# Kernel optimization log

Measured on AMD Instinct MI355X. Metric: run time of the kernel, lower is better.

The kernel has to match this reference:

```python
import jax, jax.numpy as jnp
import numpy as np

FONT_NUM = 190
HID = 256
HEADS = 2
EPS = 1e-5


def _bn(x, g, b, m, v):
    # eval-mode BatchNorm over the last (channel) axis
    return (x - m) * (g * jax.lax.rsqrt(v + EPS)) + b


def _gru(x, Wih, Whh, bih, bhh):
    # x: [B, S, D]; PyTorch gate order r, z, n. Returns all hidden states [B, S, H].
    B, S, _ = x.shape
    H = Whh.shape[1]
    xp = x @ Wih.T + bih  # [B, S, 3H] -- one big GEMM for all timesteps
    def step(h, xt):
        gh = h @ Whh.T + bhh
        xr, xz, xn = jnp.split(xt, 3, axis=-1)
        hr, hz, hn = jnp.split(gh, 3, axis=-1)
        r = jax.nn.sigmoid(xr + hr)
        z = jax.nn.sigmoid(xz + hz)
        n = jnp.tanh(xn + r * hn)
        h_new = (1.0 - z) * n + z * h
        return h_new, h_new
    h0 = jnp.zeros((B, H), x.dtype)
    _, hs = jax.lax.scan(step, h0, jnp.swapaxes(xp, 0, 1))
    return jnp.swapaxes(hs, 0, 1)


def _forward(img_emb, text_embs, len_mask, label_mask, labels,
             img_W, img_b, img_g, img_beta, img_m, img_v,
             g1_Wih, g1_Whh, g1_bih, g1_bhh, tl_W, tl_b,
             t_g, t_beta, t_m, t_v,
             g2_Wih, g2_Whh, g2_bih, g2_bhh, cl_W, cl_b,
             c_g, c_beta, c_m, c_v,
             attn_Win, attn_bin, attn_Wout, attn_bout, pred_W, pred_b):
    # img encoder: Linear -> BN -> (Dropout eval=id) -> ReLU
    img_fea = jax.nn.relu(_bn(img_emb @ img_W.T + img_b, img_g, img_beta, img_m, img_v))  # [B,H]
    # text encoder: GRU -> ReLU -> Linear, then BN+ReLU (torch does this in [B,C,S]; equivalent over channels)
    t = jax.nn.relu(_gru(text_embs, g1_Wih, g1_Whh, g1_bih, g1_bhh))
    t = t @ tl_W.T + tl_b
    text_fea = jax.nn.relu(_bn(t, t_g, t_beta, t_m, t_v))  # [B,S,H]
    len_info = len_mask.sum(axis=1)  # [B]
    # NOTE: sum over ALL timesteps divided by valid length (faithful to source)
    mean = text_fea.sum(axis=1) / len_info[:, None]  # [B,H]
    contrast = text_fea - mean[:, None, :]
    c = jax.nn.relu(_gru(contrast, g2_Wih, g2_Whh, g2_bih, g2_bhh))
    c = c @ cl_W.T + cl_b
    contrast_fea = jax.nn.relu(_bn(c, c_g, c_beta, c_m, c_v))  # [B,S,H]
    B, S, H = text_fea.shape
    hd = H // HEADS
    # batched 3-token self-attention: collapse the per-timestep python loop into one call
    tokens = jnp.stack([
        jnp.broadcast_to(img_fea[:, None, :], (B, S, H)), text_fea, contrast_fea
    ], axis=0).reshape(3, B * S, H)  # [3, N, H]
    Wq, Wk, Wv = jnp.split(attn_Win, 3, axis=0)
    bq, bk, bv = jnp.split(attn_bin, 3, axis=0)
    scale = 1.0 / jnp.sqrt(jnp.asarray(hd, tokens.dtype))
    q = (tokens @ Wq.T + bq).reshape(3, B * S, HEADS, hd) * scale
    k = (tokens @ Wk.T + bk).reshape(3, B * S, HEADS, hd)
    v = (tokens @ Wv.T + bv).reshape(3, B * S, HEADS, hd)
    scores = jnp.einsum('tnhd,snhd->nhts', q, k)  # [N, heads, 3, 3]
    attn = jax.nn.softmax(scores, axis=-1)
    o = jnp.einsum('nhts,snhd->tnhd', attn, v).reshape(3, B * S, H)
    o = o @ attn_Wout.T + attn_bout
    last = o.mean(axis=0).reshape(B, S, H)  # att_fea.mean(0) over the 3 tokens
    logits = last @ pred_W.T + pred_b  # [B,S,FONT_NUM]
    pred = jax.nn.softmax(logits, axis=-1)
    oh = jnp.maximum(label_mask, jax.nn.one_hot(labels, FONT_NUM, dtype=pred.dtype))
    loss = -(oh * jnp.log(pred)).sum(axis=-1)  # [B,S]
    loss = (loss * len_mask).sum(axis=1) / len_info
    return loss.mean()


def setup_inputs() -> dict:
    key = jax.random.key(0)
    ks = jax.random.split(key, 16)
    B, S, D, H = 128, 128, 2048, HID
    img_emb = jax.random.normal(ks[0], (B, D), jnp.float32)
    text_embs = jax.random.normal(ks[1], (B, S, D), jnp.float32)
    lengths = jax.random.randint(ks[2], (B,), S // 2, S + 1)
    len_mask = (jnp.arange(S)[None, :] < lengths[:, None]).astype(jnp.float32)
    labels = jax.random.randint(ks[3], (B, S), 0, FONT_NUM)
    label_mask = jnp.zeros((B, S, FONT_NUM), jnp.float32)
    w = lambda k, sh: jax.random.normal(k, sh, jnp.float32) * 0.02
    params = dict(
        img_W=w(ks[4], (H, D)), img_b=jnp.zeros((H,)),
        img_g=jnp.ones((H,)), img_beta=jnp.zeros((H,)), img_m=jnp.zeros((H,)), img_v=jnp.ones((H,)),
        g1_Wih=w(ks[5], (3 * (H // 2), D)), g1_Whh=w(ks[6], (3 * (H // 2), H // 2)),
        g1_bih=jnp.zeros((3 * (H // 2),)), g1_bhh=jnp.zeros((3 * (H // 2),)),
        tl_W=w(ks[7], (H, H // 2)), tl_b=jnp.zeros((H,)),
        t_g=jnp.ones((H,)), t_beta=jnp.zeros((H,)), t_m=jnp.zeros((H,)), t_v=jnp.ones((H,)),
        g2_Wih=w(ks[8], (3 * H, H)), g2_Whh=w(ks[9], (3 * H, H)),
        g2_bih=jnp.zeros((3 * H,)), g2_bhh=jnp.zeros((3 * H,)),
        cl_W=w(ks[10], (H, H)), cl_b=jnp.zeros((H,)),
        c_g=jnp.ones((H,)), c_beta=jnp.zeros((H,)), c_m=jnp.zeros((H,)), c_v=jnp.ones((H,)),
        attn_Win=w(ks[11], (3 * H, H)), attn_bin=jnp.zeros((3 * H,)),
        attn_Wout=w(ks[12], (H, H)), attn_bout=jnp.zeros((H,)),
        pred_W=w(ks[13], (FONT_NUM, H)), pred_b=jnp.zeros((FONT_NUM,)),
    )
    return dict(img_emb=img_emb, text_embs=text_embs, len_mask=len_mask,
                label_mask=label_mask, labels=labels, **params)


def reference(img_emb, text_embs, len_mask, label_mask, labels,
              img_W, img_b, img_g, img_beta, img_m, img_v,
              g1_Wih, g1_Whh, g1_bih, g1_bhh, tl_W, tl_b,
              t_g, t_beta, t_m, t_v,
              g2_Wih, g2_Whh, g2_bih, g2_bhh, cl_W, cl_b,
              c_g, c_beta, c_m, c_v,
              attn_Win, attn_bin, attn_Wout, attn_bout, pred_W, pred_b):
    return _forward(img_emb, text_embs, len_mask, label_mask, labels,
                    img_W, img_b, img_g, img_beta, img_m, img_v,
                    g1_Wih, g1_Whh, g1_bih, g1_bhh, tl_W, tl_b,
                    t_g, t_beta, t_m, t_v,
                    g2_Wih, g2_Whh, g2_bih, g2_bhh, cl_W, cl_b,
                    c_g, c_beta, c_m, c_v,
                    attn_Win, attn_bin, attn_Wout, attn_bout, pred_W, pred_b)
```

## Files before the change

### kernel.cpp

```cpp
#include <hip/hip_runtime.h>

typedef __attribute__((ext_vector_type(8))) short short8;
typedef __attribute__((ext_vector_type(4))) float f32x4;
typedef _Float16 f16;
typedef __attribute__((ext_vector_type(2))) _Float16 f16x2;
typedef __attribute__((ext_vector_type(8))) _Float16 f16x8;

__device__ inline float bf2f(unsigned short u){
  union{float f; unsigned u32;} x; x.u32 = ((unsigned)u) << 16; return x.f;
}
__device__ inline unsigned short f2bf(float f){
  union{float f; unsigned u;} x; x.f = f;
  unsigned r = (x.u + 0x7FFFu + ((x.u >> 16) & 1u)) >> 16;
  return (unsigned short)r;
}

#if defined(__has_builtin)
#  if __has_builtin(__builtin_amdgcn_fdot2)
#    define HAS_FDOT2 1
#  endif
#endif
__device__ inline float dot2f(f16x2 a, f16x2 b, float c){
#ifdef HAS_FDOT2
  return __builtin_amdgcn_fdot2(a, b, c, false);
#else
  return c + (float)a.x * (float)b.x + (float)a.y * (float)b.y;
#endif
}
__device__ inline f16x2 asf16x2(int v){ return __builtin_bit_cast(f16x2, v); }
__device__ inline int pack2(float lo, float hi){
  f16x2 p = f16x2{(f16)lo, (f16)hi};
  return __builtin_bit_cast(int, p);
}

__device__ inline float sigmoidf_(float x){ return 1.f / (1.f + __expf(-x)); }
__device__ inline float tanh_fast(float x){ float e = __expf(2.f * x); return 1.f - 2.f / (e + 1.f); }

__device__ inline float dpp_xor1(float x){
  return __int_as_float(__builtin_amdgcn_update_dpp(0, __float_as_int(x), 0xB1, 0xF, 0xF, true));
}
__device__ inline float dpp_xor2(float x){
  return __int_as_float(__builtin_amdgcn_update_dpp(0, __float_as_int(x), 0x4E, 0xF, 0xF, true));
}

__device__ inline void load8bf(const unsigned short* p, float* o){
  uint4 q = *(const uint4*)p;
  o[0]=bf2f((unsigned short)(q.x & 0xffffu)); o[1]=bf2f((unsigned short)(q.x >> 16));
  o[2]=bf2f((unsigned short)(q.y & 0xffffu)); o[3]=bf2f((unsigned short)(q.y >> 16));
  o[4]=bf2f((unsigned short)(q.z & 0xffffu)); o[5]=bf2f((unsigned short)(q.z >> 16));
  o[6]=bf2f((unsigned short)(q.w & 0xffffu)); o[7]=bf2f((unsigned short)(q.w >> 16));
}

#define GLL16(g, l) __builtin_amdgcn_global_load_lds(                      \
    (const __attribute__((address_space(1))) void*)(g),                    \
    (__attribute__((address_space(3))) void*)(l), 16, 0, 0)

__global__ __launch_bounds__(256) void conv_bf16_k(const float* __restrict__ src,
                                                   unsigned short* __restrict__ dst, int n4){
  int i = blockIdx.x * 256 + threadIdx.x;
  if (i >= n4) return;
  float4 v = ((const float4*)src)[i];
  union { unsigned short s[4]; uint2 q; } u;
  u.s[0]=f2bf(v.x); u.s[1]=f2bf(v.y); u.s[2]=f2bf(v.z); u.s[3]=f2bf(v.w);
  ((uint2*)dst)[i] = u.q;
}

__global__ __launch_bounds__(256) void pred_pad_k(const float* __restrict__ W,
                                                  const float* __restrict__ b,
                                                  unsigned short* __restrict__ Wd,
                                                  float* __restrict__ bd){
  int i = blockIdx.x * 256 + threadIdx.x;
  int j = i >> 8;
  Wd[i] = (j < 190) ? f2bf(W[i]) : (unsigned short)0;
  if (i < 192) bd[i] = (i < 190) ? b[i] : 0.f;
}

template<int OUT_T, bool BN, bool AF32>
__global__ __launch_bounds__(256) void gemm128_k(
    const void* __restrict__ Ap, const unsigned short* __restrict__ Bw,
    const float* __restrict__ bias,
    const float* __restrict__ gam, const float* __restrict__ bet,
    const float* __restrict__ mu,  const float* __restrict__ var,
    void* __restrict__ Cp, int M, int N, int K)
{
  __shared__ __align__(16) unsigned short As[4096];
  __shared__ __align__(16) unsigned short Bs[4096];
  const int tid  = threadIdx.x;
  const int lane = tid & 63, wid = tid >> 6;
  const int wm = wid & 1, wn = wid >> 1;
  const int bm = blockIdx.y << 7, bn = blockIdx.x << 7;
  const int rA = tid >> 2, seg = tid & 3;

  f32x4 acc[4][4];
  #pragma unroll
  for (int i = 0; i < 4; i++)
    #pragma unroll
    for (int j = 0; j < 4; j++)
      acc[i][j] = f32x4{0.f, 0.f, 0.f, 0.f};

  const unsigned short* Abf = (const unsigned short*)Ap;
  const float* Af = (const float*)Ap;
  char* asb = (char*)As;
  char* bsb = (char*)Bs;
  char* asw = asb + wid * 1024;
  char* bsw = bsb + wid * 1024;

  for (int k0 = 0; k0 < K; k0 += 32) {
    if (AF32) {
      #pragma unroll
      for (int beta = 0; beta < 2; beta++) {
        const float* src = Af + (size_t)(bm + rA + beta * 64) * K + k0 + seg * 8;
        float4 v0 = *(const float4*)src;
        float4 v1 = *(const float4*)(src + 4);
        union { unsigned short s[8]; uint4 q; } u;
        u.s[0]=f2bf(v0.x); u.s[1]=f2bf(v0.y); u.s[2]=f2bf(v0.z); u.s[3]=f2bf(v0.w);
        u.s[4]=f2bf(v1.x); u.s[5]=f2bf(v1.y); u.s[6]=f2bf(v1.z); u.s[7]=f2bf(v1.w);
        *(uint4*)(asb + beta * 4096 + tid * 16) = u.q;
      }
    } else {
      GLL16(Abf + (size_t)(bm + rA)      * K + k0 + seg * 8, asw);
      GLL16(Abf + (size_t)(bm + rA + 64) * K + k0 + seg * 8, asw + 4096);
    }
    GLL16(Bw + (size_t)(bn + rA)      * K + k0 + seg * 8, bsw);
    GLL16(Bw + (size_t)(bn + rA + 64) * K + k0 + seg * 8, bsw + 4096);
    __syncthreads();

    short8 a[4], b[4];
    #pragma unroll
    for (int f = 0; f < 4; f++) {
      int ra = wm * 64 + f * 16 + (lane & 15);
      a[f] = *(const short8*)(asb + ra * 64 + (lane >> 4) * 16);
      int rb = wn * 64 + f * 16 + (lane & 15);
      b[f] = *(const short8*)(bsb + rb * 64 + (lane >> 4) * 16);
    }
    #pragma unroll
    for (int fm = 0; fm < 4; fm++)
      #pragma unroll
      for (int fn = 0; fn < 4; fn++)
        acc[fm][fn] = __builtin_amdgcn_mfma_f32_16x16x32_bf16(a[fm], b[fn], acc[fm][fn], 0, 0, 0);
    __syncthreads();
  }

  #pragma unroll
  for (int fn = 0; fn < 4; fn++) {
    int col = bn + wn * 64 + fn * 16 + (lane & 15);
    float bs = bias[col];
    float sc = 1.f, sh = 0.f;
    if (BN) { float s = gam[col] * rsqrtf(var[col] + 1e-5f); sc = s; sh = bet[col] - mu[col] * s; }
    #pragma unroll
    for (int fm = 0; fm < 4; fm++) {
      int row = bm + wm * 64 + fm * 16 + ((lane >> 4) << 2);
      #pragma unroll
      for (int j = 0; j < 4; j++) {
        float v = acc[fm][fn][j] + bs;
        if (BN) { v = v * sc + sh; v = fmaxf(v, 0.f); }
        size_t idx = (size_t)(row + j) * N + col;
        if (OUT_T == 1) ((f16*)Cp)[idx] = (f16)v;
        else            ((unsigned short*)Cp)[idx] = f2bf(v);
      }
    }
  }
}

template<int OUT_T, bool BN, bool AF32>
__global__ __launch_bounds__(256) void gemm_k(
    const void* __restrict__ Ap, const unsigned short* __restrict__ Bw,
    const float* __restrict__ bias,
    const float* __restrict__ gam, const float* __restrict__ bet,
    const float* __restrict__ mu,  const float* __restrict__ var,
    void* __restrict__ Cp, int M, int N, int K)
{
  __shared__ unsigned short As[64][40];
  __shared__ unsigned short Bs[64][40];
  const int tid  = threadIdx.x;
  const int lane = tid & 63, wid = tid >> 6;
  const int wm = wid & 1, wn = wid >> 1;
  const int bm = blockIdx.y << 6, bn = blockIdx.x << 6;
  const int srow = tid >> 2, sseg = tid & 3;

  f32x4 acc[2][2];
  #pragma unroll
  for (int i = 0; i < 2; i++)
    #pragma unroll
    for (int j = 0; j < 2; j++)
      acc[i][j] = f32x4{0.f, 0.f, 0.f, 0.f};

  const unsigned short* Abf = (const unsigned short*)Ap;
  const float* Af = (const float*)Ap;

  for (int k0 = 0; k0 < K; k0 += 32) {
    if (AF32) {
      const float* src = Af + (size_t)(bm + srow) * K + k0 + sseg * 8;
      float4 v0 = *(const float4*)(src);
      float4 v1 = *(const float4*)(src + 4);
      union { unsigned short s[8]; uint4 q; } u;
      u.s[0]=f2bf(v0.x); u.s[1]=f2bf(v0.y); u.s[2]=f2bf(v0.z); u.s[3]=f2bf(v0.w);
      u.s[4]=f2bf(v1.x); u.s[5]=f2bf(v1.y); u.s[6]=f2bf(v1.z); u.s[7]=f2bf(v1.w);
      *(uint4*)&As[srow][sseg * 8] = u.q;
    } else {
      *(uint4*)&As[srow][sseg * 8] =
          *(const uint4*)(Abf + (size_t)(bm + srow) * K + k0 + sseg * 8);
    }
    *(uint4*)&Bs[srow][sseg * 8] =
        *(const uint4*)(Bw + (size_t)(bn + srow) * K + k0 + sseg * 8);
    __syncthreads();

    short8 a0 = *(const short8*)&As[wm * 32 +      (lane & 15)][(lane >> 4) * 8];
    short8 a1 = *(const short8*)&As[wm * 32 + 16 + (lane & 15)][(lane >> 4) * 8];
    short8 b0 = *(const short8*)&Bs[wn * 32 +      (lane & 15)][(lane >> 4) * 8];
    short8 b1 = *(const short8*)&Bs[wn * 32 + 16 + (lane & 15)][(lane >> 4) * 8];
    acc[0][0] = __builtin_amdgcn_mfma_f32_16x16x32_bf16(a0, b0, acc[0][0], 0, 0, 0);
    acc[0][1] = __builtin_amdgcn_mfma_f32_16x16x32_bf16(a0, b1, acc[0][1], 0, 0, 0);
    acc[1][0] = __builtin_amdgcn_mfma_f32_16x16x32_bf16(a1, b0, acc[1][0], 0, 0, 0);
    acc[1][1] = __builtin_amdgcn_mfma_f32_16x16x32_bf16(a1, b1, acc[1][1], 0, 0, 0);
    __syncthreads();
  }

  #pragma unroll
  for (int fn = 0; fn < 2; fn++) {
    int col = bn + wn * 32 + fn * 16 + (lane & 15);
    float bs = bias[col];
    float sc = 1.f, sh = 0.f;
    if (BN) { float s = gam[col] * rsqrtf(var[col] + 1e-5f); sc = s; sh = bet[col] - mu[col] * s; }
    #pragma unroll
    for (int fm = 0; fm < 2; fm++) {
      int row = bm + wm * 32 + fm * 16 + ((lane >> 4) << 2);
      #pragma unroll
      for (int j = 0; j < 4; j++) {
        float v = acc[fm][fn][j] + bs;
        if (BN) { v = v * sc + sh; v = fmaxf(v, 0.f); }
        size_t idx = (size_t)(row + j) * N + col;
        if (OUT_T == 0)      ((float*)Cp)[idx] = v;
        else if (OUT_T == 1) ((f16*)Cp)[idx]   = (f16)v;
        else                 ((unsigned short*)Cp)[idx] = f2bf(v);
      }
    }
  }
}

__global__ __launch_bounds__(512, 2) void gru2_scan_k(
    const float* __restrict__ Whh, const float* __restrict__ bhh,
    const f16* __restrict__ xp, unsigned short* __restrict__ hs_relu)
{
  const int b = blockIdx.x;
  const int tid = threadIdx.x;
  const int jj = tid >> 1, kh = tid & 1;
  __shared__ __align__(16) f16 hbuf[2][256];

  int wri[64], wzi[64], wni[64];
  #pragma unroll
  for (int i = 0; i < 16; i++) {
    const int kb = kh * 128 + i * 8;
    float4 f0, f1;
    f0 = *(const float4*)&Whh[(size_t)(jj      ) * 256 + kb];
    f1 = *(const float4*)&Whh[(size_t)(jj      ) * 256 + kb + 4];
    wri[4*i+0] = pack2(f0.x, f0.y); wri[4*i+1] = pack2(f0.z, f0.w);
    wri[4*i+2] = pack2(f1.x, f1.y); wri[4*i+3] = pack2(f1.z, f1.w);
    f0 = *(const float4*)&Whh[(size_t)(jj + 256) * 256 + kb];
    f1 = *(const float4*)&Whh[(size_t)(jj + 256) * 256 + kb + 4];
    wzi[4*i+0] = pack2(f0.x, f0.y); wzi[4*i+1] = pack2(f0.z, f0.w);
    wzi[4*i+2] = pack2(f1.x, f1.y); wzi[4*i+3] = pack2(f1.z, f1.w);
    f0 = *(const float4*)&Whh[(size_t)(jj + 512) * 256 + kb];
    f1 = *(const float4*)&Whh[(size_t)(jj + 512) * 256 + kb + 4];
    wni[4*i+0] = pack2(f0.x, f0.y); wni[4*i+1] = pack2(f0.z, f0.w);
    wni[4*i+2] = pack2(f1.x, f1.y); wni[4*i+3] = pack2(f1.z, f1.w);
  }
  #pragma unroll
  for (int i = 0; i < 64; i++)
    asm volatile("" : "+v"(wri[i]), "+v"(wzi[i]), "+v"(wni[i]));

  const float br = bhh[jj], bz = bhh[jj + 256], bn2 = bhh[jj + 512];
  if (tid < 256) hbuf[0][tid] = (f16)0.f;
  float hprev = 0.f;
  f16 pxr = (f16)0.f, pxz = (f16)0.f, pxn = (f16)0.f;
  if (kh == 0) {
    const f16* x0 = xp + (size_t)(b * 128) * 768;
    pxr = x0[jj]; pxz = x0[256 + jj]; pxn = x0[512 + jj];
  }
  __syncthreads();
  int cur = 0;
  for (int t = 0; t < 128; t++) {
    float xr = (float)pxr, xz = (float)pxz, xn = (float)pxn;
    if (kh == 0) {
      const int tn = (t < 127) ? (t + 1) : 127;
      const f16* xnr = xp + (size_t)(b * 128 + tn) * 768;
      pxr = xnr[jj]; pxz = xnr[256 + jj]; pxn = xnr[512 + jj];
    }
    const char* hb = (const char*)hbuf[cur] + kh * 256;
    float ar = 0.f, az = 0.f, an = 0.f;
    #pragma unroll
    for (int c = 0; c < 16; c++) {
      f16x8 hv = *(const f16x8*)(hb + c * 16);
      #pragma unroll
      for (int u = 0; u < 4; u++) {
        f16x2 hp = f16x2{hv[2*u], hv[2*u+1]};
        ar = dot2f(asf16x2(wri[4*c+u]), hp, ar);
        az = dot2f(asf16x2(wzi[4*c+u]), hp, az);
        an = dot2f(asf16x2(wni[4*c+u]), hp, an);
      }
    }
    ar += dpp_xor1(ar);
    az += dpp_xor1(az);
    an += dpp_xor1(an);
    if (kh == 0) {
      float r = sigmoidf_(xr + ar + br);
      float z = sigmoidf_(xz + az + bz);
      float n = tanh_fast(xn + r * (an + bn2));
      float hnew = (1.f - z) * n + z * hprev;
      hprev = hnew;
      hbuf[cur ^ 1][jj] = (f16)hnew;
      hs_relu[(size_t)(b * 128 + t) * 256 + jj] = f2bf(fmaxf(hnew, 0.f));
    }
    __syncthreads();
    cur ^= 1;
  }
}

__global__ __launch_bounds__(512, 4) void gru1_scan_k(
    const float* __restrict__ Whh, const float* __restrict__ bhh,
    const f16* __restrict__ xp, unsigned short* __restrict__ hs_relu)
{
  const int b = blockIdx.x;
  const int tid = threadIdx.x;
  const int jj = tid >> 2, kh = tid & 3;
  __shared__ __align__(16) f16 hbuf[2][128];

  int wri[16], wzi[16], wni[16];
  #pragma unroll
  for (int i = 0; i < 4; i++) {
    const int kb = kh * 32 + i * 8;
    float4 f0, f1;
    f0 = *(const float4*)&Whh[(size_t)(jj      ) * 128 + kb];
    f1 = *(const float4*)&Whh[(size_t)(jj      ) * 128 + kb + 4];
    wri[4*i+0] = pack2(f0.x, f0.y); wri[4*i+1] = pack2(f0.z, f0.w);
    wri[4*i+2] = pack2(f1.x, f1.y); wri[4*i+3] = pack2(f1.z, f1.w);
    f0 = *(const float4*)&Whh[(size_t)(jj + 128) * 128 + kb];
    f1 = *(const float4*)&Whh[(size_t)(jj + 128) * 128 + kb + 4];
    wzi[4*i+0] = pack2(f0.x, f0.y); wzi[4*i+1] = pack2(f0.z, f0.w);
    wzi[4*i+2] = pack2(f1.x, f1.y); wzi[4*i+3] = pack2(f1.z, f1.w);
    f0 = *(const float4*)&Whh[(size_t)(jj + 256) * 128 + kb];
    f1 = *(const float4*)&Whh[(size_t)(jj + 256) * 128 + kb + 4];
    wni[4*i+0] = pack2(f0.x, f0.y); wni[4*i+1] = pack2(f0.z, f0.w);
    wni[4*i+2] = pack2(f1.x, f1.y); wni[4*i+3] = pack2(f1.z, f1.w);
  }
  #pragma unroll
  for (int i = 0; i < 16; i++)
    asm volatile("" : "+v"(wri[i]), "+v"(wzi[i]), "+v"(wni[i]));

  const float br = bhh[jj], bz = bhh[jj + 128], bn2 = bhh[jj + 256];
  if (tid < 128) hbuf[0][tid] = (f16)0.f;
  float hprev = 0.f;
  f16 pxr = (f16)0.f, pxz = (f16)0.f, pxn = (f16)0.f;
  if (kh == 0) {
    const f16* x0 = xp + (size_t)(b * 128) * 384;
    pxr = x0[jj]; pxz = x0[128 + jj]; pxn = x0[256 + jj];
  }
  __syncthreads();
  int cur = 0;
  for (int t = 0; t < 128; t++) {
    float xr = (float)pxr, xz = (float)pxz, xn = (float)pxn;
    if (kh == 0) {
      const int tn = (t < 127) ? (t + 1) : 127;
      const f16* xnr = xp + (size_t)(b * 128 + tn) * 384;
      pxr = xnr[jj]; pxz = xnr[128 + jj]; pxn = xnr[256 + jj];
    }
    const char* hb = (const char*)hbuf[cur] + kh * 64;
    float ar = 0.f, az = 0.f, an = 0.f;
    #pragma unroll
    for (int c = 0; c < 4; c++) {
      f16x8 hv = *(const f16x8*)(hb + c * 16);
      #pragma unroll
      for (int u = 0; u < 4; u++) {
        f16x2 hp = f16x2{hv[2*u], hv[2*u+1]};
        ar = dot2f(asf16x2(wri[4*c+u]), hp, ar);
        az = dot2f(asf16x2(wzi[4*c+u]), hp, az);
        an = dot2f(asf16x2(wni[4*c+u]), hp, an);
      }
    }
    ar += dpp_xor1(ar); ar += dpp_xor2(ar);
    az += dpp_xor1(az); az += dpp_xor2(az);
    an += dpp_xor1(an); an += dpp_xor2(an);
    if (kh == 0) {
      float r = sigmoidf_(xr + ar + br);
      float z = sigmoidf_(xz + az + bz);
      float n = tanh_fast(xn + r * (an + bn2));
      float hnew = (1.f - z) * n + z * hprev;
      hprev = hnew;
      hbuf[cur ^ 1][jj] = (f16)hnew;
      hs_relu[(size_t)(b * 128 + t) * 128 + jj] = f2bf(fmaxf(hnew, 0.f));
    }
    __syncthreads();
    cur ^= 1;
  }
}

__global__ __launch_bounds__(256) void mean_k(const unsigned short* __restrict__ tf,
                                              const float* __restrict__ len_mask,
                                              float* __restrict__ mean,
                                              float* __restrict__ len_info){
  int b = blockIdx.x, c = threadIdx.x;
  float acc = 0.f;
  for (int s = 0; s < 128; s++) acc += bf2f(tf[(size_t)(b * 128 + s) * 256 + c]);
  float len = 0.f;
  for (int s = 0; s < 128; s++) len += len_mask[b * 128 + s];
  mean[b * 256 + c] = acc / len;
  if (c == 0) len_info[b] = len;
}

__global__ __launch_bounds__(256) void contrast_k(const unsigned short* __restrict__ tf,
                                                  const float* __restrict__ mean,
                                                  unsigned short* __restrict__ out){
  size_t i = (size_t)blockIdx.x * 256 + threadIdx.x;
  int c = (int)(i & 255);
  int b = (int)(i >> 15);
  out[i] = f2bf(bf2f(tf[i]) - mean[b * 256 + c]);
}

__global__ __launch_bounds__(256) void attn_k(const unsigned short* __restrict__ qkv0,
                                              const unsigned short* __restrict__ qkv1,
                                              const unsigned short* __restrict__ qkv2,
                                              unsigned short* __restrict__ osum){
  int i = blockIdx.x * 256 + threadIdx.x;
  int h = i & 1; int n = i >> 1; int b = n >> 7;
  const unsigned short* t0 = qkv0 + (size_t)b * 768 + h * 128;
  const unsigned short* t1 = qkv1 + (size_t)n * 768 + h * 128;
  const unsigned short* t2 = qkv2 + (size_t)n * 768 + h * 128;
  float sc[3][3];
  #pragma unroll
  for (int a = 0; a < 3; a++)
    #pragma unroll
    for (int s = 0; s < 3; s++) sc[a][s] = 0.f;
  #pragma unroll 1
  for (int dc = 0; dc < 16; dc++) {
    float q[3][8], k[3][8];
    load8bf(t0 + dc * 8, q[0]); load8bf(t1 + dc * 8, q[1]); load8bf(t2 + dc * 8, q[2]);
    load8bf(t0 + 256 + dc * 8, k[0]); load8bf(t1 + 256 + dc * 8, k[1]); load8bf(t2 + 256 + dc * 8, k[2]);
    #pragma unroll
    for (int a = 0; a < 3; a++)
      #pragma unroll
      for (int s = 0; s < 3; s++) {
        float d = 0.f;
        #pragma unroll
        for (int e = 0; e < 8; e++) d += q[a][e] * k[s][e];
        sc[a][s] += d;
      }
  }
  const float scale = 0.08838834764831845f;
  float w[3] = {0.f, 0.f, 0.f};
  #pragma unroll
  for (int a = 0; a < 3; a++) {
    float s0 = sc[a][0] * scale, s1 = sc[a][1] * scale, s2 = sc[a][2] * scale;
    float m = fmaxf(s0, fmaxf(s1, s2));
    float e0 = __expf(s0 - m), e1 = __expf(s1 - m), e2 = __expf(s2 - m);
    float inv = 1.f / (e0 + e1 + e2);
    w[0] += e0 * inv; w[1] += e1 * inv; w[2] += e2 * inv;
  }
  w[0] *= (1.f / 3.f); w[1] *= (1.f / 3.f); w[2] *= (1.f / 3.f);
  unsigned short* op = osum + (size_t)n * 256 + h * 128;
  #pragma unroll 1
  for (int dc = 0; dc < 16; dc++) {
    float v0[8], v1[8], v2[8];
    load8bf(t0 + 512 + dc * 8, v0); load8bf(t1 + 512 + dc * 8, v1); load8bf(t2 + 512 + dc * 8, v2);
    union { unsigned short s[8]; uint4 q; } u;
    #pragma unroll
    for (int e = 0; e < 8; e++) u.s[e] = f2bf(w[0] * v0[e] + w[1] * v1[e] + w[2] * v2[e]);
    *(uint4*)(op + dc * 8) = u.q;
  }
}

__global__ __launch_bounds__(64) void loss_k(const float* __restrict__ logits,
                                             const float* __restrict__ label_mask,
                                             const int* __restrict__ labels,
                                             float* __restrict__ loss_raw){
  int r = blockIdx.x; int j = threadIdx.x;
  int lab = labels[r];
  float l[3]; float m = -1e30f;
  #pragma unroll
  for (int q = 0; q < 3; q++) {
    int c = j + q * 64;
    float lv = (c < 190) ? logits[(size_t)r * 192 + c] : -1e30f;
    l[q] = lv; m = fmaxf(m, lv);
  }
  #pragma unroll
  for (int off = 32; off; off >>= 1) m = fmaxf(m, __shfl_xor(m, off));
  float se = 0.f, soh = 0.f, dot = 0.f;
  #pragma unroll
  for (int q = 0; q < 3; q++) {
    int c = j + q * 64;
    if (c < 190) {
      se += expf(l[q] - m);
      float oh = fmaxf(label_mask[(size_t)r * 190 + c], (c == lab) ? 1.f : 0.f);
      soh += oh; dot += oh * l[q];
    }
  }
  #pragma unroll
  for (int off = 32; off; off >>= 1) {
    se += __shfl_xor(se, off); soh += __shfl_xor(soh, off); dot += __shfl_xor(dot, off);
  }
  if (j == 0) loss_raw[r] = (m + logf(se)) * soh - dot;
}

__global__ __launch_bounds__(256) void final_k(const float* __restrict__ loss_raw,
                                               const float* __restrict__ len_mask,
                                               const float* __restrict__ len_info,
                                               float* __restrict__ out){
  __shared__ float sh[256];
  int t = threadIdx.x;
  float acc = 0.f;
  for (int i = t; i < 16384; i += 256) acc += loss_raw[i] * len_mask[i] / len_info[i >> 7];
  sh[t] = acc; __syncthreads();
  for (int s = 128; s; s >>= 1) { if (t < s) sh[t] += sh[t + s]; __syncthreads(); }
  if (t == 0) out[0] = sh[0] / 128.f;
}

extern "C" void kernel_launch(void* const* d_in, const int* in_sizes, int n_in,
                              void* d_out, int out_size, void* d_ws, size_t ws_size,
                              hipStream_t stream)
{
  const float* img_emb    = (const float*)d_in[0];
  const float* text_embs  = (const float*)d_in[1];
  const float* len_mask   = (const float*)d_in[2];
  const float* label_mask = (const float*)d_in[3];
  const int*   labels     = (const int*)  d_in[4];
  const float* img_W   = (const float*)d_in[5];
  const float* img_b   = (const float*)d_in[6];
  const float* img_g   = (const float*)d_in[7];
  const float* img_be  = (const float*)d_in[8];
  const float* img_m   = (const float*)d_in[9];
  const float* img_v   = (const float*)d_in[10];
  const float* g1_Wih  = (const float*)d_in[11];
  const float* g1_Whh  = (const float*)d_in[12];
  const float* g1_bih  = (const float*)d_in[13];
  const float* g1_bhh  = (const float*)d_in[14];
  const float* tl_W    = (const float*)d_in[15];
  const float* tl_b    = (const float*)d_in[16];
  const float* t_g     = (const float*)d_in[17];
  const float* t_be    = (const float*)d_in[18];
  const float* t_m     = (const float*)d_in[19];
  const float* t_v     = (const float*)d_in[20];
  const float* g2_Wih  = (const float*)d_in[21];
  const float* g2_Whh  = (const float*)d_in[22];
  const float* g2_bih  = (const float*)d_in[23];
  const float* g2_bhh  = (const float*)d_in[24];
  const float* cl_W    = (const float*)d_in[25];
  const float* cl_b    = (const float*)d_in[26];
  const float* c_g     = (const float*)d_in[27];
  const float* c_be    = (const float*)d_in[28];
  const float* c_m     = (const float*)d_in[29];
  const float* c_v     = (const float*)d_in[30];
  const float* a_Win   = (const float*)d_in[31];
  const float* a_bin   = (const float*)d_in[32];
  const float* a_Wout  = (const float*)d_in[33];
  const float* a_bout  = (const float*)d_in[34];
  const float* pred_W  = (const float*)d_in[35];
  const float* pred_b  = (const float*)d_in[36];

  char* ws = (char*)d_ws;
  size_t o = 0;
  auto alloc = [&](size_t sz){ size_t r = o; o += (sz + 255) & ~(size_t)255; return r; };

  size_t o_g1Wih = alloc(384ull*2048*2);
  size_t o_tlW   = alloc(256ull*128*2);
  size_t o_g2Wih = alloc(768ull*256*2);
  size_t o_clW   = alloc(256ull*256*2);
  size_t o_aWin  = alloc(768ull*256*2);
  size_t o_aWout = alloc(256ull*256*2);
  size_t o_imgW  = alloc(256ull*2048*2);
  size_t o_predW = alloc(192ull*256*2);
  size_t o_predb = alloc(192ull*4);
  size_t o_imgfea= alloc(128ull*256*2);
  size_t o_mean  = alloc(128ull*256*4);
  size_t o_len   = alloc(128ull*4);
  size_t o_R0    = alloc(33554432ull);
  size_t o_RB    = alloc(25165824ull);
  size_t o_tfea  = alloc(16384ull*256*2);
  size_t o_qkv1  = alloc(16384ull*768*2);
  size_t o_cfea  = alloc(16384ull*256*2);
  size_t o_qkv0  = alloc(128ull*768*2);
  size_t o_loss  = alloc(16384ull*4);
  (void)ws_size; (void)in_sizes; (void)n_in; (void)out_size;

  unsigned short* g1Wih_bf = (unsigned short*)(ws + o_g1Wih);
  unsigned short* tlW_bf   = (unsigned short*)(ws + o_tlW);
  unsigned short* g2Wih_bf = (unsigned short*)(ws + o_g2Wih);
  unsigned short* clW_bf   = (unsigned short*)(ws + o_clW);
  unsigned short* aWin_bf  = (unsigned short*)(ws + o_aWin);
  unsigned short* aWout_bf = (unsigned short*)(ws + o_aWout);
  unsigned short* imgW_bf  = (unsigned short*)(ws + o_imgW);
  unsigned short* predW_bf = (unsigned short*)(ws + o_predW);
  float*          predb_p  = (float*)(ws + o_predb);
  unsigned short* img_fea  = (unsigned short*)(ws + o_imgfea);
  float*          meanb    = (float*)(ws + o_mean);
  float*          len_info = (float*)(ws + o_len);
  f16*            xp2      = (f16*)(ws + o_R0);
  unsigned short* hs2      = (unsigned short*)(ws + o_R0 + 25165824ull);
  unsigned short* osum     = (unsigned short*)(ws + o_R0);
  unsigned short* lastb    = (unsigned short*)(ws + o_R0 + 8388608ull);
  f16*            xp1      = (f16*)(ws + o_RB);
  unsigned short* hs1      = (unsigned short*)(ws + o_RB + 12582912ull);
  unsigned short* contr    = (unsigned short*)(ws + o_RB + 16777216ull);
  unsigned short* qkv2     = (unsigned short*)(ws + o_RB);
  unsigned short* tfea     = (unsigned short*)(ws + o_tfea);
  unsigned short* qkv1     = (unsigned short*)(ws + o_qkv1);
  float*          logits   = (float*)(ws + o_qkv1);
  unsigned short* cfea     = (unsigned short*)(ws + o_cfea);
  unsigned short* qkv0     = (unsigned short*)(ws + o_qkv0);
  float*          loss_raw = (float*)(ws + o_loss);
  float*          outp     = (float*)d_out;

  conv_bf16_k<<<768, 256, 0, stream>>>(g1_Wih, g1Wih_bf, 196608);
  conv_bf16_k<<<32,  256, 0, stream>>>(tl_W,   tlW_bf,   8192);
  conv_bf16_k<<<192, 256, 0, stream>>>(g2_Wih, g2Wih_bf, 49152);
  conv_bf16_k<<<64,  256, 0, stream>>>(cl_W,   clW_bf,   16384);
  conv_bf16_k<<<192, 256, 0, stream>>>(a_Win,  aWin_bf,  49152);
  conv_bf16_k<<<64,  256, 0, stream>>>(a_Wout, aWout_bf, 16384);
  conv_bf16_k<<<512, 256, 0, stream>>>(img_W,  imgW_bf,  131072);
  pred_pad_k<<<192, 256, 0, stream>>>(pred_W, pred_b, predW_bf, predb_p);

  gemm128_k<2, true, true><<<dim3(2, 1), 256, 0, stream>>>(
      img_emb, imgW_bf, img_b, img_g, img_be, img_m, img_v, img_fea, 128, 256, 2048);

  gemm128_k<1, false, true><<<dim3(3, 128), 256, 0, stream>>>(
      text_embs, g1Wih_bf, g1_bih, nullptr, nullptr, nullptr, nullptr, xp1, 16384, 384, 2048);

  gru1_scan_k<<<128, 512, 0, stream>>>(g1_Whh, g1_bhh, xp1, hs1);

  gemm128_k<2, true, false><<<dim3(2, 128), 256, 0, stream>>>(
      hs1, tlW_bf, tl_b, t_g, t_be, t_m, t_v, tfea, 16384, 256, 128);

  mean_k<<<128, 256, 0, stream>>>(tfea, len_mask, meanb, len_info);
  contrast_k<<<16384, 256, 0, stream>>>(tfea, meanb, contr);

  gemm128_k<1, false, false><<<dim3(6, 128), 256, 0, stream>>>(
      contr, g2Wih_bf, g2_bih, nullptr, nullptr, nullptr, nullptr, xp2, 16384, 768, 256);

  gru2_scan_k<<<128, 512, 0, stream>>>(g2_Whh, g2_bhh, xp2, hs2);

  gemm128_k<2, true, false><<<dim3(2, 128), 256, 0, stream>>>(
      hs2, clW_bf, cl_b, c_g, c_be, c_m, c_v, cfea, 16384, 256, 256);

  gemm128_k<2, false, false><<<dim3(6, 1), 256, 0, stream>>>(
      img_fea, aWin_bf, a_bin, nullptr, nullptr, nullptr, nullptr, qkv0, 128, 768, 256);
  gemm128_k<2, false, false><<<dim3(6, 128), 256, 0, stream>>>(
      tfea, aWin_bf, a_bin, nullptr, nullptr, nullptr, nullptr, qkv1, 16384, 768, 256);
  gemm128_k<2, false, false><<<dim3(6, 128), 256, 0, stream>>>(
      cfea, aWin_bf, a_bin, nullptr, nullptr, nullptr, nullptr, qkv2, 16384, 768, 256);

  attn_k<<<128, 256, 0, stream>>>(qkv0, qkv1, qkv2, osum);

  gemm128_k<2, false, false><<<dim3(2, 128), 256, 0, stream>>>(
      osum, aWout_bf, a_bout, nullptr, nullptr, nullptr, nullptr, lastb, 16384, 256, 256);

  gemm_k<0, false, false><<<dim3(3, 256), 256, 0, stream>>>(
      lastb, predW_bf, predb_p, nullptr, nullptr, nullptr, nullptr, logits, 16384, 192, 256);

  loss_k<<<16384, 64, 0, stream>>>(logits, label_mask, labels, loss_raw);
  final_k<<<1, 256, 0, stream>>>(loss_raw, len_mask, len_info, outp);
}
```

Measured before the change: 638.7 us.

## Split second GRU scan reduction across four lanes per hidden unit

```diff
diff --git a/kernel.cpp b/kernel.cpp
--- a/kernel.cpp
+++ b/kernel.cpp
@@ -62,6 +62,16 @@
   float4 v = ((const float4*)src)[i];
   union { unsigned short s[4]; uint2 q; } u;
   u.s[0]=f2bf(v.x); u.s[1]=f2bf(v.y); u.s[2]=f2bf(v.z); u.s[3]=f2bf(v.w);
+  ((uint2*)dst)[i] = u.q;
+}
+
+__global__ __launch_bounds__(256) void conv_f16_k(const float* __restrict__ src,
+                                                  f16* __restrict__ dst, int n4){
+  int i = blockIdx.x * 256 + threadIdx.x;
+  if (i >= n4) return;
+  float4 v = ((const float4*)src)[i];
+  union { f16 s[4]; uint2 q; } u;
+  u.s[0]=(f16)v.x; u.s[1]=(f16)v.y; u.s[2]=(f16)v.z; u.s[3]=(f16)v.w;
   ((uint2*)dst)[i] = u.q;
 }
 
@@ -238,35 +248,31 @@
   }
 }
 
-__global__ __launch_bounds__(512, 2) void gru2_scan_k(
-    const float* __restrict__ Whh, const float* __restrict__ bhh,
-    const f16* __restrict__ xp, unsigned short* __restrict__ hs_relu)
+__global__ __launch_bounds__(1024) __attribute__((amdgpu_waves_per_eu(4, 4)))
+void gru2_scan_k(const f16* __restrict__ Wf,
+                 const float* __restrict__ bhh,
+                 const f16* __restrict__ xp, unsigned short* __restrict__ hs_relu)
 {
   const int b = blockIdx.x;
   const int tid = threadIdx.x;
-  const int jj = tid >> 1, kh = tid & 1;
+  const int jj = tid >> 2, kh = tid & 3;
   __shared__ __align__(16) f16 hbuf[2][256];
 
-  int wri[64], wzi[64], wni[64];
-  #pragma unroll
-  for (int i = 0; i < 16; i++) {
-    const int kb = kh * 128 + i * 8;
-    float4 f0, f1;
-    f0 = *(const float4*)&Whh[(size_t)(jj      ) * 256 + kb];
-    f1 = *(const float4*)&Whh[(size_t)(jj      ) * 256 + kb + 4];
-    wri[4*i+0] = pack2(f0.x, f0.y); wri[4*i+1] = pack2(f0.z, f0.w);
-    wri[4*i+2] = pack2(f1.x, f1.y); wri[4*i+3] = pack2(f1.z, f1.w);
-    f0 = *(const float4*)&Whh[(size_t)(jj + 256) * 256 + kb];
-    f1 = *(const float4*)&Whh[(size_t)(jj + 256) * 256 + kb + 4];
-    wzi[4*i+0] = pack2(f0.x, f0.y); wzi[4*i+1] = pack2(f0.z, f0.w);
-    wzi[4*i+2] = pack2(f1.x, f1.y); wzi[4*i+3] = pack2(f1.z, f1.w);
-    f0 = *(const float4*)&Whh[(size_t)(jj + 512) * 256 + kb];
-    f1 = *(const float4*)&Whh[(size_t)(jj + 512) * 256 + kb + 4];
-    wni[4*i+0] = pack2(f0.x, f0.y); wni[4*i+1] = pack2(f0.z, f0.w);
-    wni[4*i+2] = pack2(f1.x, f1.y); wni[4*i+3] = pack2(f1.z, f1.w);
-  }
-  #pragma unroll
-  for (int i = 0; i < 64; i++)
+  int wri[32], wzi[32], wni[32];
+  #pragma unroll
+  for (int i = 0; i < 8; i++) {
+    const int cc = (i + 2 * kh) & 7;
+    const int kb = kh * 64 + cc * 8;
+    uint4 q;
+    q = *(const uint4*)&Wf[(size_t)(jj      ) * 256 + kb];
+    wri[4*i+0] = (int)q.x; wri[4*i+1] = (int)q.y; wri[4*i+2] = (int)q.z; wri[4*i+3] = (int)q.w;
+    q = *(const uint4*)&Wf[(size_t)(jj + 256) * 256 + kb];
+    wzi[4*i+0] = (int)q.x; wzi[4*i+1] = (int)q.y; wzi[4*i+2] = (int)q.z; wzi[4*i+3] = (int)q.w;
+    q = *(const uint4*)&Wf[(size_t)(jj + 512) * 256 + kb];
+    wni[4*i+0] = (int)q.x; wni[4*i+1] = (int)q.y; wni[4*i+2] = (int)q.z; wni[4*i+3] = (int)q.w;
+  }
+  #pragma unroll
+  for (int i = 0; i < 32; i++)
     asm volatile("" : "+v"(wri[i]), "+v"(wzi[i]), "+v"(wni[i]));
 
   const float br = bhh[jj], bz = bhh[jj + 256], bn2 = bhh[jj + 512];
@@ -286,22 +292,23 @@
       const f16* xnr = xp + (size_t)(b * 128 + tn) * 768;
       pxr = xnr[jj]; pxz = xnr[256 + jj]; pxn = xnr[512 + jj];
     }
-    const char* hb = (const char*)hbuf[cur] + kh * 256;
+    const char* hb = (const char*)hbuf[cur] + kh * 128;
     float ar = 0.f, az = 0.f, an = 0.f;
     #pragma unroll
-    for (int c = 0; c < 16; c++) {
-      f16x8 hv = *(const f16x8*)(hb + c * 16);
+    for (int i = 0; i < 8; i++) {
+      const int cc = (i + 2 * kh) & 7;
+      f16x8 hv = *(const f16x8*)(hb + cc * 16);
       #pragma unroll
       for (int u = 0; u < 4; u++) {
         f16x2 hp = f16x2{hv[2*u], hv[2*u+1]};
-        ar = dot2f(asf16x2(wri[4*c+u]), hp, ar);
-        az = dot2f(asf16x2(wzi[4*c+u]), hp, az);
-        an = dot2f(asf16x2(wni[4*c+u]), hp, an);
+        ar = dot2f(asf16x2(wri[4*i+u]), hp, ar);
+        az = dot2f(asf16x2(wzi[4*i+u]), hp, az);
+        an = dot2f(asf16x2(wni[4*i+u]), hp, an);
       }
     }
-    ar += dpp_xor1(ar);
-    az += dpp_xor1(az);
-    an += dpp_xor1(an);
+    ar += dpp_xor1(ar); ar += dpp_xor2(ar);
+    az += dpp_xor1(az); az += dpp_xor2(az);
+    an += dpp_xor1(an); an += dpp_xor2(an);
     if (kh == 0) {
       float r = sigmoidf_(xr + ar + br);
       float z = sigmoidf_(xz + az + bz);
@@ -562,6 +569,7 @@
   size_t o_g1Wih = alloc(384ull*2048*2);
   size_t o_tlW   = alloc(256ull*128*2);
   size_t o_g2Wih = alloc(768ull*256*2);
+  size_t o_g2Whh = alloc(768ull*256*2);
   size_t o_clW   = alloc(256ull*256*2);
   size_t o_aWin  = alloc(768ull*256*2);
   size_t o_aWout = alloc(256ull*256*2);
@@ -583,6 +591,7 @@
   unsigned short* g1Wih_bf = (unsigned short*)(ws + o_g1Wih);
   unsigned short* tlW_bf   = (unsigned short*)(ws + o_tlW);
   unsigned short* g2Wih_bf = (unsigned short*)(ws + o_g2Wih);
+  f16*            g2Whh_f  = (f16*)(ws + o_g2Whh);
   unsigned short* clW_bf   = (unsigned short*)(ws + o_clW);
   unsigned short* aWin_bf  = (unsigned short*)(ws + o_aWin);
   unsigned short* aWout_bf = (unsigned short*)(ws + o_aWout);
@@ -611,6 +620,7 @@
   conv_bf16_k<<<768, 256, 0, stream>>>(g1_Wih, g1Wih_bf, 196608);
   conv_bf16_k<<<32,  256, 0, stream>>>(tl_W,   tlW_bf,   8192);
   conv_bf16_k<<<192, 256, 0, stream>>>(g2_Wih, g2Wih_bf, 49152);
+  conv_f16_k <<<192, 256, 0, stream>>>(g2_Whh, g2Whh_f,  49152);
   conv_bf16_k<<<64,  256, 0, stream>>>(cl_W,   clW_bf,   16384);
   conv_bf16_k<<<192, 256, 0, stream>>>(a_Win,  aWin_bf,  49152);
   conv_bf16_k<<<64,  256, 0, stream>>>(a_Wout, aWout_bf, 16384);
@@ -634,7 +644,7 @@
   gemm128_k<1, false, false><<<dim3(6, 128), 256, 0, stream>>>(
       contr, g2Wih_bf, g2_bih, nullptr, nullptr, nullptr, nullptr, xp2, 16384, 768, 256);
 
-  gru2_scan_k<<<128, 512, 0, stream>>>(g2_Whh, g2_bhh, xp2, hs2);
+  gru2_scan_k<<<128, 1024, 0, stream>>>(g2Whh_f, g2_bhh, xp2, hs2);
 
   gemm128_k<2, true, false><<<dim3(2, 128), 256, 0, stream>>>(
       hs2, clW_bf, cl_b, c_g, c_be, c_m, c_v, cfea, 16384, 256, 256);
```

After: 723.6 us. +13.3%, slower.
